# Kernel tuning notes

Measured on AMD Instinct MI355X. Metric: run time of the kernel, lower is better.

## Reference

```python
import jax, jax.numpy as jnp
import numpy as np

NEG_INF = -1e15  # matches masked_fill value -1000000000000000.0
ALPHA = 0.2      # leakyReLU negative slope


def setup_inputs() -> dict:
    key = jax.random.key(0)
    k1, k2, k3, k4 = jax.random.split(key, 4)
    N, F_IN, F_OUT = 8192, 256, 64
    x = jax.random.normal(k1, (N, F_IN), dtype=jnp.float32)
    mask = jax.random.randint(k2, (N, N), 0, 2, dtype=jnp.int32)
    trans = jax.random.normal(k3, (F_IN, F_OUT), dtype=jnp.float32) * 0.1
    attn = jax.random.normal(k4, (2 * F_OUT, 1), dtype=jnp.float32) * 0.1
    return {"x": x, "mask": mask, "trans": trans, "attn": attn}


def reference(x, mask, trans, attn):
    d = trans.shape[1]
    h = x @ trans                                  # [N, d]
    e1 = h @ attn[:d, :]                           # [N, 1]
    e2 = h @ attn[d:, :]                           # [N, 1]
    scores = jax.nn.leaky_relu(e1 + e2.T, negative_slope=ALPHA)  # [N, N]
    masked = jnp.where(mask == 0, NEG_INF, scores)
    attention = jax.nn.softmax(masked, axis=1)
    return attention @ h                           # [N, d]
```

## Files before the change

kernel.cpp:

```cpp
#include <hip/hip_runtime.h>
#include <hip/hip_bf16.h>
#include <math.h>

#define N 8192
#define FIN 256
#define D 64
#define ALPHA 0.2f

typedef __attribute__((ext_vector_type(8))) short bf16x8;
typedef __attribute__((ext_vector_type(4))) float f32x4;

__global__ __launch_bounds__(256) void k_h_e(
    const float* __restrict__ x, const float* __restrict__ trans,
    const float* __restrict__ attn,
    __hip_bfloat16* __restrict__ hT, float* __restrict__ e1, float* __restrict__ e2)
{
    __shared__ float xs[8 * FIN];
    __shared__ __hip_bfloat16 hl[8 * D];
    const int t = threadIdx.x;
    const int r0 = blockIdx.x * 8;

    #pragma unroll
    for (int v = 0; v < 2; ++v) {
        int idx = t + 256 * v;
        ((float4*)xs)[idx] = ((const float4*)(x + (size_t)r0 * FIN))[idx];
    }
    __syncthreads();

    const int lane = t & 63, w = t >> 6;
    const float* xa = xs + (2 * w) * FIN;
    const float* xb = xs + (2 * w + 1) * FIN;
    float acca = 0.f, accb = 0.f;
    #pragma unroll 8
    for (int k = 0; k < FIN; ++k) {
        const float tv = trans[k * D + lane];
        acca = fmaf(xa[k], tv, acca);
        accb = fmaf(xb[k], tv, accb);
    }
    const int ra = r0 + 2 * w, rb = ra + 1;

    const float a1 = attn[lane], a2 = attn[D + lane];
    float p1a = acca * a1, p2a = acca * a2;
    float p1b = accb * a1, p2b = accb * a2;
    #pragma unroll
    for (int mm = 1; mm <= 32; mm <<= 1) {
        p1a += __shfl_xor(p1a, mm);
        p2a += __shfl_xor(p2a, mm);
        p1b += __shfl_xor(p1b, mm);
        p2b += __shfl_xor(p2b, mm);
    }
    if (lane == 0) { e1[ra] = p1a; e2[ra] = p2a; e1[rb] = p1b; e2[rb] = p2b; }

    hl[(2 * w) * D + lane]     = __float2bfloat16(acca);
    hl[(2 * w + 1) * D + lane] = __float2bfloat16(accb);
    __syncthreads();
    if (t < D) {
        union { bf16x8 v; __hip_bfloat16 h[8]; } o;
        #pragma unroll
        for (int r = 0; r < 8; ++r) o.h[r] = hl[r * D + t];
        *(bf16x8*)(hT + (size_t)t * N + r0) = o.v;
    }
}

__global__ __launch_bounds__(256) void k_attn(
    const int* __restrict__ mask, const __hip_bfloat16* __restrict__ hT,
    const float* __restrict__ e1, const float* __restrict__ e2,
    float* __restrict__ acc_part, float* __restrict__ l_part, int cs)
{
    const int t = threadIdx.x;
    const int lane = t & 63, wave = t >> 6;
    const int i0 = (blockIdx.y * 4 + wave) * 16;
    const int sp = blockIdx.x;
    const int c0 = sp * cs;
    const int m = lane & 15, quad = lane >> 4;
    const int row = i0 + m;
    const float er = e1[row];
    const size_t mrow = (size_t)row * N;

    f32x4 acc0 = {0.f, 0.f, 0.f, 0.f};
    f32x4 acc1 = {0.f, 0.f, 0.f, 0.f};
    f32x4 acc2 = {0.f, 0.f, 0.f, 0.f};
    f32x4 acc3 = {0.f, 0.f, 0.f, 0.f};
    float lsum = 0.f;

    const __hip_bfloat16* hb0 = hT + (size_t)(m     ) * N;
    const __hip_bfloat16* hb1 = hT + (size_t)(m + 16) * N;
    const __hip_bfloat16* hb2 = hT + (size_t)(m + 32) * N;
    const __hip_bfloat16* hb3 = hT + (size_t)(m + 48) * N;

    #pragma unroll 2
    for (int j = c0; j < c0 + cs; j += 32) {
        const int jb = j + quad * 8;
        const int4   m0 = *(const int4*)(mask + mrow + jb);
        const int4   m1 = *(const int4*)(mask + mrow + jb + 4);
        const float4 ea = *(const float4*)(e2 + jb);
        const float4 eb = *(const float4*)(e2 + jb + 4);
        const bf16x8 b0 = *(const bf16x8*)(hb0 + jb);
        const bf16x8 b1 = *(const bf16x8*)(hb1 + jb);
        const bf16x8 b2 = *(const bf16x8*)(hb2 + jb);
        const bf16x8 b3 = *(const bf16x8*)(hb3 + jb);

        float s0 = er + ea.x; s0 = s0 > 0.f ? s0 : ALPHA * s0;
        float s1 = er + ea.y; s1 = s1 > 0.f ? s1 : ALPHA * s1;
        float s2 = er + ea.z; s2 = s2 > 0.f ? s2 : ALPHA * s2;
        float s3 = er + ea.w; s3 = s3 > 0.f ? s3 : ALPHA * s3;
        float s4 = er + eb.x; s4 = s4 > 0.f ? s4 : ALPHA * s4;
        float s5 = er + eb.y; s5 = s5 > 0.f ? s5 : ALPHA * s5;
        float s6 = er + eb.z; s6 = s6 > 0.f ? s6 : ALPHA * s6;
        float s7 = er + eb.w; s7 = s7 > 0.f ? s7 : ALPHA * s7;
        const float p0 = m0.x ? __expf(s0) : 0.f;
        const float p1 = m0.y ? __expf(s1) : 0.f;
        const float p2 = m0.z ? __expf(s2) : 0.f;
        const float p3 = m0.w ? __expf(s3) : 0.f;
        const float p4 = m1.x ? __expf(s4) : 0.f;
        const float p5 = m1.y ? __expf(s5) : 0.f;
        const float p6 = m1.z ? __expf(s6) : 0.f;
        const float p7 = m1.w ? __expf(s7) : 0.f;

        union { bf16x8 v; __hip_bfloat162 h2[4]; } af;
        af.h2[0] = __float22bfloat162_rn(make_float2(p0, p1));
        af.h2[1] = __float22bfloat162_rn(make_float2(p2, p3));
        af.h2[2] = __float22bfloat162_rn(make_float2(p4, p5));
        af.h2[3] = __float22bfloat162_rn(make_float2(p6, p7));

        lsum += ((p0 + p1) + (p2 + p3)) + ((p4 + p5) + (p6 + p7));

        acc0 = __builtin_amdgcn_mfma_f32_16x16x32_bf16(af.v, b0, acc0, 0, 0, 0);
        acc1 = __builtin_amdgcn_mfma_f32_16x16x32_bf16(af.v, b1, acc1, 0, 0, 0);
        acc2 = __builtin_amdgcn_mfma_f32_16x16x32_bf16(af.v, b2, acc2, 0, 0, 0);
        acc3 = __builtin_amdgcn_mfma_f32_16x16x32_bf16(af.v, b3, acc3, 0, 0, 0);
    }

    lsum += __shfl_xor(lsum, 16);
    lsum += __shfl_xor(lsum, 32);
    if (quad == 0) l_part[(size_t)sp * N + row] = lsum;

    #pragma unroll
    for (int reg = 0; reg < 4; ++reg) {
        const size_t rbase = ((size_t)sp * N + i0 + quad * 4 + reg) * D;
        acc_part[rbase + m     ] = acc0[reg];
        acc_part[rbase + m + 16] = acc1[reg];
        acc_part[rbase + m + 32] = acc2[reg];
        acc_part[rbase + m + 48] = acc3[reg];
    }
}

__global__ __launch_bounds__(256) void k_reduce(
    const float* __restrict__ acc_part, const float* __restrict__ l_part,
    float* __restrict__ out, int nsplit)
{
    const int idx = blockIdx.x * 256 + threadIdx.x;
    const int row = idx >> 6;
    float sum = 0.f, l = 0.f;
    for (int s = 0; s < nsplit; ++s) {
        sum += acc_part[(size_t)s * N * D + idx];
        l   += l_part[(size_t)s * N + row];
    }
    out[idx] = sum / l;
}

extern "C" void kernel_launch(void* const* d_in, const int* in_sizes, int n_in,
                              void* d_out, int out_size, void* d_ws, size_t ws_size,
                              hipStream_t stream) {
    const float* x     = (const float*)d_in[0];
    const int*   mask  = (const int*)d_in[1];
    const float* trans = (const float*)d_in[2];
    const float* attn  = (const float*)d_in[3];
    float* out = (float*)d_out;

    char* ws = (char*)d_ws;
    __hip_bfloat16* hT = (__hip_bfloat16*)ws;
    float* e1 = (float*)(ws + (size_t)D * N * sizeof(__hip_bfloat16));
    float* e2 = e1 + N;
    float* l_part = e2 + N;

    const size_t base = (size_t)D * N * sizeof(__hip_bfloat16)
                      + 2 * (size_t)N * sizeof(float);
    int nsplit = 1;
    const int cands[4] = {8, 4, 2, 1};
    for (int ci = 0; ci < 4; ++ci) {
        int s = cands[ci];
        size_t need = base + (size_t)s * N * sizeof(float)
                    + (size_t)s * N * D * sizeof(float);
        if (need <= ws_size) { nsplit = s; break; }
    }
    float* acc_part = l_part + (size_t)nsplit * N;

    k_h_e<<<N / 8, 256, 0, stream>>>(x, trans, attn, hT, e1, e2);
    dim3 g2(nsplit, N / 64);
    k_attn<<<g2, 256, 0, stream>>>(mask, hT, e1, e2, acc_part, l_part, N / nsplit);
    k_reduce<<<(N * D) / 256, 256, 0, stream>>>(acc_part, l_part, out, nsplit);
}
```

Baseline: 437.6 us.

## Pack mask into bitmask in pre-pass and software-pipeline attention loop loads

Adds a pre-pass kernel that compresses the int32 mask into one bit per element, so the attention kernel reads 1 byte per 8 columns instead of 32 bytes. The attention loop is also restructured to prefetch the next iteration's mask byte, e2 values and hT fragments before computing the current one. The full int32 mask still has to be read once by the pack kernel, which adds a launch and a bitmask write. The prefetch also reads one step past the end of each split's column range.

```diff
diff --git a/kernel.cpp b/kernel.cpp
--- a/kernel.cpp
+++ b/kernel.cpp
@@ -9,6 +9,19 @@
 
 typedef __attribute__((ext_vector_type(8))) short bf16x8;
 typedef __attribute__((ext_vector_type(4))) float f32x4;
+
+__global__ __launch_bounds__(256) void k_pack(
+    const int* __restrict__ mask, unsigned char* __restrict__ mp)
+{
+    const size_t t = (size_t)blockIdx.x * 256 + threadIdx.x;
+    const int4* s = (const int4*)mask + 2 * t;
+    const int4 a = s[0], b = s[1];
+    unsigned v = (a.x != 0 ? 1u : 0u) | (a.y != 0 ? 2u : 0u)
+               | (a.z != 0 ? 4u : 0u) | (a.w != 0 ? 8u : 0u)
+               | (b.x != 0 ? 16u : 0u) | (b.y != 0 ? 32u : 0u)
+               | (b.z != 0 ? 64u : 0u) | (b.w != 0 ? 128u : 0u);
+    mp[t] = (unsigned char)v;
+}
 
 __global__ __launch_bounds__(256) void k_h_e(
     const float* __restrict__ x, const float* __restrict__ trans,
@@ -63,7 +76,7 @@
 }
 
 __global__ __launch_bounds__(256) void k_attn(
-    const int* __restrict__ mask, const __hip_bfloat16* __restrict__ hT,
+    const unsigned char* __restrict__ mp, const __hip_bfloat16* __restrict__ hT,
     const float* __restrict__ e1, const float* __restrict__ e2,
     float* __restrict__ acc_part, float* __restrict__ l_part, int cs)
 {
@@ -75,7 +88,8 @@
     const int m = lane & 15, quad = lane >> 4;
     const int row = i0 + m;
     const float er = e1[row];
-    const size_t mrow = (size_t)row * N;
+
+    const unsigned char* mb = mp + ((size_t)row << 10) + (c0 >> 3) + quad;
 
     f32x4 acc0 = {0.f, 0.f, 0.f, 0.f};
     f32x4 acc1 = {0.f, 0.f, 0.f, 0.f};
@@ -88,17 +102,26 @@
     const __hip_bfloat16* hb2 = hT + (size_t)(m + 32) * N;
     const __hip_bfloat16* hb3 = hT + (size_t)(m + 48) * N;
 
-    #pragma unroll 2
-    for (int j = c0; j < c0 + cs; j += 32) {
-        const int jb = j + quad * 8;
-        const int4   m0 = *(const int4*)(mask + mrow + jb);
-        const int4   m1 = *(const int4*)(mask + mrow + jb + 4);
-        const float4 ea = *(const float4*)(e2 + jb);
-        const float4 eb = *(const float4*)(e2 + jb + 4);
-        const bf16x8 b0 = *(const bf16x8*)(hb0 + jb);
-        const bf16x8 b1 = *(const bf16x8*)(hb1 + jb);
-        const bf16x8 b2 = *(const bf16x8*)(hb2 + jb);
-        const bf16x8 b3 = *(const bf16x8*)(hb3 + jb);
+    const int jb0 = c0 + quad * 8;
+    const int iters = cs >> 5;
+
+    unsigned mc = mb[0];
+    float4 ea = *(const float4*)(e2 + jb0);
+    float4 eb = *(const float4*)(e2 + jb0 + 4);
+    bf16x8 b0 = *(const bf16x8*)(hb0 + jb0);
+    bf16x8 b1 = *(const bf16x8*)(hb1 + jb0);
+    bf16x8 b2 = *(const bf16x8*)(hb2 + jb0);
+    bf16x8 b3 = *(const bf16x8*)(hb3 + jb0);
+
+    for (int it = 0; it < iters; ++it) {
+        const int jn = jb0 + (it + 1) * 32;
+        const unsigned mn = mb[(it + 1) * 4];
+        const float4 na = *(const float4*)(e2 + jn);
+        const float4 nb = *(const float4*)(e2 + jn + 4);
+        const bf16x8 n0 = *(const bf16x8*)(hb0 + jn);
+        const bf16x8 n1 = *(const bf16x8*)(hb1 + jn);
+        const bf16x8 n2 = *(const bf16x8*)(hb2 + jn);
+        const bf16x8 n3 = *(const bf16x8*)(hb3 + jn);
 
         float s0 = er + ea.x; s0 = s0 > 0.f ? s0 : ALPHA * s0;
         float s1 = er + ea.y; s1 = s1 > 0.f ? s1 : ALPHA * s1;
@@ -108,14 +131,14 @@
         float s5 = er + eb.y; s5 = s5 > 0.f ? s5 : ALPHA * s5;
         float s6 = er + eb.z; s6 = s6 > 0.f ? s6 : ALPHA * s6;
         float s7 = er + eb.w; s7 = s7 > 0.f ? s7 : ALPHA * s7;
-        const float p0 = m0.x ? __expf(s0) : 0.f;
-        const float p1 = m0.y ? __expf(s1) : 0.f;
-        const float p2 = m0.z ? __expf(s2) : 0.f;
-        const float p3 = m0.w ? __expf(s3) : 0.f;
-        const float p4 = m1.x ? __expf(s4) : 0.f;
-        const float p5 = m1.y ? __expf(s5) : 0.f;
-        const float p6 = m1.z ? __expf(s6) : 0.f;
-        const float p7 = m1.w ? __expf(s7) : 0.f;
+        const float p0 = (mc & 1u)   ? __expf(s0) : 0.f;
+        const float p1 = (mc & 2u)   ? __expf(s1) : 0.f;
+        const float p2 = (mc & 4u)   ? __expf(s2) : 0.f;
+        const float p3 = (mc & 8u)   ? __expf(s3) : 0.f;
+        const float p4 = (mc & 16u)  ? __expf(s4) : 0.f;
+        const float p5 = (mc & 32u)  ? __expf(s5) : 0.f;
+        const float p6 = (mc & 64u)  ? __expf(s6) : 0.f;
+        const float p7 = (mc & 128u) ? __expf(s7) : 0.f;
 
         union { bf16x8 v; __hip_bfloat162 h2[4]; } af;
         af.h2[0] = __float22bfloat162_rn(make_float2(p0, p1));
@@ -129,6 +152,8 @@
         acc1 = __builtin_amdgcn_mfma_f32_16x16x32_bf16(af.v, b1, acc1, 0, 0, 0);
         acc2 = __builtin_amdgcn_mfma_f32_16x16x32_bf16(af.v, b2, acc2, 0, 0, 0);
         acc3 = __builtin_amdgcn_mfma_f32_16x16x32_bf16(af.v, b3, acc3, 0, 0, 0);
+
+        mc = mn; ea = na; eb = nb; b0 = n0; b1 = n1; b2 = n2; b3 = n3;
     }
 
     lsum += __shfl_xor(lsum, 16);
@@ -170,24 +195,25 @@
 
     char* ws = (char*)d_ws;
     __hip_bfloat16* hT = (__hip_bfloat16*)ws;
-    float* e1 = (float*)(ws + (size_t)D * N * sizeof(__hip_bfloat16));
-    float* e2 = e1 + N;
-    float* l_part = e2 + N;
-
-    const size_t base = (size_t)D * N * sizeof(__hip_bfloat16)
-                      + 2 * (size_t)N * sizeof(float);
+    char* p = ws + (size_t)D * N * sizeof(__hip_bfloat16);
+    float* e1 = (float*)p;            p += (size_t)N * sizeof(float);
+    float* e2 = (float*)p;            p += (size_t)N * sizeof(float);
+    unsigned char* mp = (unsigned char*)p;  p += (size_t)N * (N / 8);
+    const size_t used = (size_t)(p - ws);
     int nsplit = 1;
     const int cands[4] = {8, 4, 2, 1};
     for (int ci = 0; ci < 4; ++ci) {
         int s = cands[ci];
-        size_t need = base + (size_t)s * N * sizeof(float)
-                    + (size_t)s * N * D * sizeof(float);
+        size_t need = used + (size_t)s * N * sizeof(float)
+                    + (size_t)s * N * D * sizeof(float) + 4096;
         if (need <= ws_size) { nsplit = s; break; }
     }
+    float* l_part = (float*)p;
     float* acc_part = l_part + (size_t)nsplit * N;
 
+    k_pack<<<(N / 16) * (N / 128), 256, 0, stream>>>(mask, mp);
     k_h_e<<<N / 8, 256, 0, stream>>>(x, trans, attn, hT, e1, e2);
     dim3 g2(nsplit, N / 64);
-    k_attn<<<g2, 256, 0, stream>>>(mask, hT, e1, e2, acc_part, l_part, N / nsplit);
+    k_attn<<<g2, 256, 0, stream>>>(mp, hT, e1, e2, acc_part, l_part, N / nsplit);
     k_reduce<<<(N * D) / 256, 256, 0, stream>>>(acc_part, l_part, out, nsplit);
 }
```

Measured after the change: 461.7 us. +5.5%, slower.
